# Optimization experiments

Measured on AMD Instinct MI355X. Metric: run time of the kernel, lower is better.

Reference implementation:

```python
import jax, jax.numpy as jnp
import numpy as np

TGT, BSZ, E = 2048, 4, 1024
NUM_HEADS = 16
HEAD_DIM = E // NUM_HEADS


def setup_inputs() -> dict:
    key = jax.random.key(0)
    ks = jax.random.split(key, 5)
    return {
        "query": jax.random.normal(ks[0], (TGT, BSZ, E), dtype=jnp.float32),
        "key": jax.random.normal(ks[1], (TGT, BSZ, E), dtype=jnp.float32),
        "value": jax.random.normal(ks[2], (TGT, BSZ, E), dtype=jnp.float32),
        "in_proj_weight": jax.random.normal(ks[3], (3 * E, E), dtype=jnp.float32) * (1.0 / np.sqrt(E)),
        "in_proj_bias": jnp.zeros((3 * E,), dtype=jnp.float32),
        "out_proj_weight": jax.random.normal(ks[4], (E, E), dtype=jnp.float32) * (1.0 / np.sqrt(E)),
        "out_proj_bias": jnp.zeros((E,), dtype=jnp.float32),
    }


def reference(query, key, value, in_proj_weight, in_proj_bias, out_proj_weight, out_proj_bias):
    tgt_len, bsz, embed_dim = query.shape
    src_len = key.shape[0]
    h, hd = NUM_HEADS, embed_dim // NUM_HEADS

    w_q, w_k, w_v = jnp.split(in_proj_weight, 3, axis=0)
    b_q, b_k, b_v = jnp.split(in_proj_bias, 3, axis=0)
    q = query @ w_q.T + b_q   # (Nt, B, E)
    k = key @ w_k.T + b_k     # (Ns, B, E)
    v = value @ w_v.T + b_v

    # (L, B, E) -> (B*H, L, hd)
    q = q.reshape(tgt_len, bsz * h, hd).transpose(1, 0, 2)
    k = k.reshape(src_len, bsz * h, hd).transpose(1, 0, 2)
    v = v.reshape(src_len, bsz * h, hd).transpose(1, 0, 2)

    q = q / jnp.sqrt(jnp.asarray(hd, dtype=q.dtype))
    attn = jnp.einsum('bte,bse->bts', q, k)          # (B*H, Nt, Ns)
    attn = jax.nn.softmax(attn, axis=-1)
    out = jnp.einsum('bts,bse->bte', attn, v)        # (B*H, Nt, hd)

    out = out.transpose(1, 0, 2).reshape(tgt_len, bsz, embed_dim)
    out = out @ out_proj_weight.T + out_proj_bias    # (Nt, B, out_dim)

    avg_weights = attn.reshape(bsz, h, tgt_len, src_len).mean(axis=1)
    return (out, avg_weights)
```

## Files before the change

### kernel.cpp

```cpp
#include <hip/hip_runtime.h>
#include <hip/hip_bf16.h>
#include <hip/hip_fp16.h>

#define TGT 2048
#define BSZ 4
#define EMB 1024
#define NH  16
#define HD  64
#define NTOK (TGT*BSZ)
#define BH   (BSZ*NH)

typedef unsigned short u16;
typedef __attribute__((ext_vector_type(8))) short    s16x8;
typedef __attribute__((ext_vector_type(8))) _Float16 f16x8;
typedef __attribute__((ext_vector_type(2))) _Float16 f16x2;
typedef __attribute__((ext_vector_type(4))) float    f32x4;

#define MFMA_BF16(a,b,c) __builtin_amdgcn_mfma_f32_16x16x32_bf16(a,b,c,0,0,0)
#define MFMA_F16(a,b,c)  __builtin_amdgcn_mfma_f32_16x16x32_f16(a,b,c,0,0,0)

#define GLOAD_LDS16(gsrc, ldst) \
  __builtin_amdgcn_global_load_lds((const __attribute__((address_space(1))) unsigned int*)(gsrc), \
                                   (__attribute__((address_space(3))) unsigned int*)(ldst), 16, 0, 0)

__device__ __forceinline__ void split_one(float x, u16& h, u16& l) {
  __hip_bfloat16 hb = __float2bfloat16(x);
  float hf = __bfloat162float(hb);
  __hip_bfloat16 lb = __float2bfloat16(x - hf);
  h = *reinterpret_cast<u16*>(&hb);
  l = *reinterpret_cast<u16*>(&lb);
}

__global__ __launch_bounds__(256) void split_kernel(const float* __restrict__ x,
    u16* __restrict__ hi, u16* __restrict__ lo, int n4) {
  int i = blockIdx.x * 256 + threadIdx.x;
  if (i >= n4) return;
  float4 v = reinterpret_cast<const float4*>(x)[i];
  ushort4 h, l;
  split_one(v.x, h.x, l.x);
  split_one(v.y, h.y, l.y);
  split_one(v.z, h.z, l.z);
  split_one(v.w, h.w, l.w);
  reinterpret_cast<ushort4*>(hi)[i] = h;
  reinterpret_cast<ushort4*>(lo)[i] = l;
}

template<int EPI>
__global__ __launch_bounds__(256) void gemm_split(
    const u16* __restrict__ Ah, const u16* __restrict__ Al,
    const u16* __restrict__ Bh, const u16* __restrict__ Bl,
    const float* __restrict__ bias, float scale, void* __restrict__ outp, int K)
{
  __shared__ __align__(16) u16 As[128*64];
  __shared__ __align__(16) u16 Bs[128*64];
  const int tid  = threadIdx.x;
  const int bm0  = blockIdx.y * 128;
  const int bn0  = blockIdx.x * 128;
  const int wave = tid >> 6, lane = tid & 63, lr = lane & 15, lg = lane >> 4;

  f32x4 zero = {0.f, 0.f, 0.f, 0.f};
  f32x4 acc[2][8];
  #pragma unroll
  for (int i = 0; i < 2; i++)
    #pragma unroll
    for (int j = 0; j < 8; j++) acc[i][j] = zero;

  const u16* srcA[4];
  const u16* srcB[4];
  #pragma unroll
  for (int j = 0; j < 4; j++) {
    int gi  = tid + j*256;
    int row = gi >> 3;
    int lgc = (gi & 7) ^ (row & 7);
    const u16* baA = (lgc < 4) ? Ah : Al;
    const u16* baB = (lgc < 4) ? Bh : Bl;
    srcA[j] = baA + (size_t)(bm0 + row)*K + (lgc & 3)*8;
    srcB[j] = baB + (size_t)(bn0 + row)*K + (lgc & 3)*8;
  }
  char* AsB = (char*)As;
  char* BsB = (char*)Bs;
  const int ldsb = wave*1024;

  for (int kt = 0; kt < K; kt += 32) {
    __syncthreads();
    #pragma unroll
    for (int j = 0; j < 4; j++) {
      GLOAD_LDS16(srcA[j] + kt, AsB + ldsb + j*4096);
      GLOAD_LDS16(srcB[j] + kt, BsB + ldsb + j*4096);
    }
    __syncthreads();

    s16x8 ah[2], al2[2];
    #pragma unroll
    for (int mf = 0; mf < 2; mf++) {
      int row = wave*32 + mf*16 + lr;
      const char* rb = AsB + row*128;
      ah[mf]  = *(const s16x8*)(rb + (((lg    ) ^ (row & 7)) << 4));
      al2[mf] = *(const s16x8*)(rb + (((lg | 4) ^ (row & 7)) << 4));
    }
    #pragma unroll
    for (int nf = 0; nf < 8; nf++) {
      int row = nf*16 + lr;
      const char* rb = BsB + row*128;
      s16x8 bh8 = *(const s16x8*)(rb + (((lg    ) ^ (row & 7)) << 4));
      s16x8 bl8 = *(const s16x8*)(rb + (((lg | 4) ^ (row & 7)) << 4));
      #pragma unroll
      for (int mf = 0; mf < 2; mf++) {
        acc[mf][nf] = MFMA_BF16(al2[mf], bh8, acc[mf][nf]);
        acc[mf][nf] = MFMA_BF16(ah[mf],  bl8, acc[mf][nf]);
        acc[mf][nf] = MFMA_BF16(ah[mf],  bh8, acc[mf][nf]);
      }
    }
  }
  #pragma unroll
  for (int mf = 0; mf < 2; mf++)
    #pragma unroll
    for (int nf = 0; nf < 8; nf++)
      #pragma unroll
      for (int r = 0; r < 4; r++) {
        int m = bm0 + wave*32 + mf*16 + lg*4 + r;
        int n = bn0 + nf*16 + lr;
        float v = (acc[mf][nf][r] + bias[n]) * scale;
        if constexpr (EPI == 0) {
          int t = m >> 2, b = m & 3, h = n >> 6, d = n & 63;
          ((_Float16*)outp)[(size_t)((b*NH + h)*TGT + t)*HD + d] = (_Float16)v;
        } else if constexpr (EPI == 1) {
          int s = m >> 2, b = m & 3, h = n >> 6, d = n & 63;
          ((_Float16*)outp)[(size_t)((b*NH + h)*HD + d)*TGT + s] = (_Float16)v;
        } else {
          ((float*)outp)[(size_t)m*EMB + n] = v;
        }
      }
}

__global__ __launch_bounds__(256) void flash_kernel(
    const _Float16* __restrict__ Qf, const _Float16* __restrict__ Kf,
    const _Float16* __restrict__ Vt, u16* __restrict__ Oh, u16* __restrict__ Ol,
    float* __restrict__ lse)
{
  __shared__ __align__(16) _Float16 Qs[64][72];
  __shared__ __align__(16) _Float16 Ks[64][72];
  __shared__ __align__(16) _Float16 Vs[64][72];
  __shared__ __align__(16) _Float16 Ps[4][16][72];
  const int tid = threadIdx.x, wave = tid >> 6, lane = tid & 63, lr = lane & 15, lg = lane >> 4;
  const int bh = blockIdx.y, t0 = blockIdx.x * 64;
  const int b = bh >> 4, h = bh & 15;

  #pragma unroll
  for (int i = 0; i < 2; i++) {
    int c = tid + i*256, r = c >> 3, co = (c & 7) * 8;
    *(uint4*)&Qs[r][co] = *(const uint4*)&Qf[((size_t)bh*TGT + t0 + r)*HD + co];
  }
  float m_run = -1e30f, l_run = 0.f;
  f32x4 zero = {0.f, 0.f, 0.f, 0.f};
  f32x4 accO[4];
  #pragma unroll
  for (int i = 0; i < 4; i++) accO[i] = zero;

  for (int s0 = 0; s0 < TGT; s0 += 64) {
    __syncthreads();
    #pragma unroll
    for (int i = 0; i < 2; i++) {
      int c = tid + i*256, r = c >> 3, co = (c & 7) * 8;
      *(uint4*)&Ks[r][co] = *(const uint4*)&Kf[((size_t)bh*TGT + s0 + r)*HD + co];
      *(uint4*)&Vs[r][co] = *(const uint4*)&Vt[((size_t)bh*HD + r)*TGT + s0 + co];
    }
    __syncthreads();
    f32x4 sacc[4];
    #pragma unroll
    for (int sf = 0; sf < 4; sf++) sacc[sf] = zero;
    #pragma unroll
    for (int sf = 0; sf < 4; sf++)
      #pragma unroll
      for (int kf = 0; kf < 2; kf++) {
        f16x8 a = *(const f16x8*)&Ks[sf*16 + lr][kf*32 + lg*8];
        f16x8 q = *(const f16x8*)&Qs[wave*16 + lr][kf*32 + lg*8];
        sacc[sf] = MFMA_F16(a, q, sacc[sf]);
      }
    float pm = -1e30f;
    #pragma unroll
    for (int sf = 0; sf < 4; sf++)
      #pragma unroll
      for (int r = 0; r < 4; r++) pm = fmaxf(pm, sacc[sf][r]);
    pm = fmaxf(pm, __shfl_xor(pm, 16, 64));
    pm = fmaxf(pm, __shfl_xor(pm, 32, 64));
    float m_new = fmaxf(m_run, pm);
    float fsc = exp2f(m_run - m_new);
    float psum = 0.f;
    #pragma unroll
    for (int sf = 0; sf < 4; sf++)
      #pragma unroll
      for (int r = 0; r < 4; r++) {
        float p = exp2f(sacc[sf][r] - m_new);
        sacc[sf][r] = p;
        psum += p;
      }
    psum += __shfl_xor(psum, 16, 64);
    psum += __shfl_xor(psum, 32, 64);
    l_run = l_run * fsc + psum;
    m_run = m_new;
    #pragma unroll
    for (int sf = 0; sf < 4; sf++) {
      f16x2 p01 = { (_Float16)sacc[sf][0], (_Float16)sacc[sf][1] };
      f16x2 p23 = { (_Float16)sacc[sf][2], (_Float16)sacc[sf][3] };
      *(f16x2*)&Ps[wave][lr][sf*16 + lg*4]     = p01;
      *(f16x2*)&Ps[wave][lr][sf*16 + lg*4 + 2] = p23;
    }
    float fr[4];
    #pragma unroll
    for (int r = 0; r < 4; r++) fr[r] = __shfl(fsc, lg*4 + r, 64);
    #pragma unroll
    for (int df = 0; df < 4; df++) {
      accO[df][0] *= fr[0]; accO[df][1] *= fr[1];
      accO[df][2] *= fr[2]; accO[df][3] *= fr[3];
    }
    f16x8 pa0 = *(const f16x8*)&Ps[wave][lr][lg*8];
    f16x8 pa1 = *(const f16x8*)&Ps[wave][lr][32 + lg*8];
    #pragma unroll
    for (int df = 0; df < 4; df++) {
      f16x8 v0 = *(const f16x8*)&Vs[df*16 + lr][lg*8];
      f16x8 v1 = *(const f16x8*)&Vs[df*16 + lr][32 + lg*8];
      accO[df] = MFMA_F16(pa0, v0, accO[df]);
      accO[df] = MFMA_F16(pa1, v1, accO[df]);
    }
  }
  float linv = 1.f / l_run;
  float rl[4];
  #pragma unroll
  for (int r = 0; r < 4; r++) rl[r] = __shfl(linv, lg*4 + r, 64);
  #pragma unroll
  for (int df = 0; df < 4; df++)
    #pragma unroll
    for (int r = 0; r < 4; r++) {
      float o = accO[df][r] * rl[r];
      int t = t0 + wave*16 + lg*4 + r;
      int d = df*16 + lr;
      size_t idx = (size_t)(t*BSZ + b)*EMB + h*HD + d;
      u16 hh, ll;
      split_one(o, hh, ll);
      Oh[idx] = hh; Ol[idx] = ll;
    }
  if (lane < 16)
    lse[(size_t)bh*TGT + t0 + wave*16 + lane] = m_run + log2f(l_run);
}

__global__ __launch_bounds__(256) void avg_kernel(
    const _Float16* __restrict__ Qf, const _Float16* __restrict__ Kf,
    const float* __restrict__ lse, float* __restrict__ avgO)
{
  __shared__ __align__(16) _Float16 Qs[128][64];
  __shared__ __align__(16) _Float16 Ks[128][64];
  __shared__ float lses[NH][128];
  const int tid = threadIdx.x, wave = tid >> 6, lane = tid & 63, lr = lane & 15, lg = lane >> 4;

  int fid = blockIdx.x;
  int nid = (fid & 7) * 128 + (fid >> 3);
  int st = nid & 15, tt = (nid >> 4) & 15, b = nid >> 8;
  int s0 = st * 128, t0 = tt * 128;

  #pragma unroll
  for (int i = 0; i < 8; i++) {
    int idx = tid + i * 256;
    int hh = idx >> 7, t = idx & 127;
    lses[hh][t] = lse[(size_t)(b*NH + hh)*TGT + t0 + t];
  }

  f32x4 zero = {0.f, 0.f, 0.f, 0.f};
  f32x4 acc[2][8];
  #pragma unroll
  for (int i = 0; i < 2; i++)
    #pragma unroll
    for (int j = 0; j < 8; j++) acc[i][j] = zero;

  const int rQ = wave * 32;
  const int srcsub = (((lane & 7) ^ (lane >> 3)) << 4) + (lane >> 3) * 128;

  for (int h = 0; h < NH; h++) {
    __syncthreads();
    {
      const char* qb = (const char*)(Qf + ((size_t)(b*NH + h)*TGT + t0) * HD);
      const char* kb = (const char*)(Kf + ((size_t)(b*NH + h)*TGT + s0) * HD);
      const char* gb = (wave < 2) ? qb : kb;
      char* lb = (char*)((wave < 2) ? &Qs[0][0] : &Ks[0][0]);
      const int half = (wave & 1) * 8;
      #pragma unroll
      for (int j = 0; j < 8; j++) {
        int J = half + j;
        GLOAD_LDS16(gb + (size_t)J * 1024 + srcsub, lb + J * 1024);
      }
    }
    __syncthreads();

    float lsr[2][4];
    #pragma unroll
    for (int mf = 0; mf < 2; mf++)
      #pragma unroll
      for (int r = 0; r < 4; r++)
        lsr[mf][r] = lses[h][rQ + mf*16 + lg*4 + r];

    f16x8 aq[2][2];
    #pragma unroll
    for (int mf = 0; mf < 2; mf++)
      #pragma unroll
      for (int kf = 0; kf < 2; kf++) {
        int row = rQ + mf*16 + lr;
        int cb = ((kf*4 + lg) ^ (row & 7)) << 4;
        aq[mf][kf] = *(const f16x8*)((const char*)&Qs[0][0] + row*128 + cb);
      }
    #pragma unroll
    for (int nf = 0; nf < 8; nf++) {
      f32x4 s4[2] = {zero, zero};
      #pragma unroll
      for (int kf = 0; kf < 2; kf++) {
        int row = nf*16 + lr;
        int cb = ((kf*4 + lg) ^ (row & 7)) << 4;
        f16x8 bk = *(const f16x8*)((const char*)&Ks[0][0] + row*128 + cb);
        s4[0] = MFMA_F16(aq[0][kf], bk, s4[0]);
        s4[1] = MFMA_F16(aq[1][kf], bk, s4[1]);
      }
      #pragma unroll
      for (int mf = 0; mf < 2; mf++)
        #pragma unroll
        for (int r = 0; r < 4; r++)
          acc[mf][nf][r] += exp2f(s4[mf][r] - lsr[mf][r]);
    }
  }

  #pragma unroll
  for (int mf = 0; mf < 2; mf++)
    #pragma unroll
    for (int nf = 0; nf < 8; nf++)
      #pragma unroll
      for (int r = 0; r < 4; r++) {
        int t = t0 + rQ + mf*16 + lg*4 + r;
        int s = s0 + nf*16 + lr;
        avgO[((size_t)b*TGT + t)*TGT + s] = acc[mf][nf][r] * (1.f/16.f);
      }
}

extern "C" void kernel_launch(void* const* d_in, const int* in_sizes, int n_in,
                              void* d_out, int out_size, void* d_ws, size_t ws_size,
                              hipStream_t stream) {
  const float* query = (const float*)d_in[0];
  const float* key_  = (const float*)d_in[1];
  const float* value = (const float*)d_in[2];
  const float* ipw   = (const float*)d_in[3];
  const float* ipb   = (const float*)d_in[4];
  const float* opw   = (const float*)d_in[5];
  const float* opb   = (const float*)d_in[6];
  float* out = (float*)d_out;
  float* avg = out + (size_t)TGT*BSZ*EMB;

  char* ws = (char*)d_ws;
  size_t o = 0;
  auto alloc = [&](size_t bytes) { char* p = ws + o; o += bytes; return p; };
  u16* Wh  = (u16*)alloc((size_t)3*EMB*EMB*2);
  u16* Wl  = (u16*)alloc((size_t)3*EMB*EMB*2);
  u16* Woh = (u16*)alloc((size_t)EMB*EMB*2);
  u16* Wol = (u16*)alloc((size_t)EMB*EMB*2);
  u16* Xh  = (u16*)alloc((size_t)NTOK*EMB*2);
  u16* Xl  = (u16*)alloc((size_t)NTOK*EMB*2);
  _Float16* Qf = (_Float16*)alloc((size_t)NTOK*EMB*2);
  _Float16* Kf = (_Float16*)alloc((size_t)NTOK*EMB*2);
  _Float16* Vt = (_Float16*)alloc((size_t)NTOK*EMB*2);
  u16* OhA = (u16*)alloc((size_t)NTOK*EMB*2);
  u16* OlA = (u16*)alloc((size_t)NTOK*EMB*2);
  float* lseA = (float*)alloc((size_t)BH*TGT*4);
  (void)ws_size; (void)in_sizes; (void)n_in; (void)out_size;

  const float QSCALE = 0.18033688011112042f;

  split_kernel<<<3*EMB*EMB/1024, 256, 0, stream>>>(ipw, Wh, Wl, 3*EMB*EMB/4);
  split_kernel<<<EMB*EMB/1024, 256, 0, stream>>>(opw, Woh, Wol, EMB*EMB/4);

  dim3 ggrid(EMB/128, NTOK/128);
  split_kernel<<<NTOK*EMB/1024, 256, 0, stream>>>(query, Xh, Xl, NTOK*EMB/4);
  gemm_split<0><<<ggrid, 256, 0, stream>>>(Xh, Xl, Wh, Wl, ipb, QSCALE, (void*)Qf, EMB);
  split_kernel<<<NTOK*EMB/1024, 256, 0, stream>>>(key_, Xh, Xl, NTOK*EMB/4);
  gemm_split<0><<<ggrid, 256, 0, stream>>>(Xh, Xl, Wh + (size_t)EMB*EMB, Wl + (size_t)EMB*EMB,
                                           ipb + EMB, 1.0f, (void*)Kf, EMB);
  split_kernel<<<NTOK*EMB/1024, 256, 0, stream>>>(value, Xh, Xl, NTOK*EMB/4);
  gemm_split<1><<<ggrid, 256, 0, stream>>>(Xh, Xl, Wh + (size_t)2*EMB*EMB, Wl + (size_t)2*EMB*EMB,
                                           ipb + 2*EMB, 1.0f, (void*)Vt, EMB);

  flash_kernel<<<dim3(TGT/64, BH), 256, 0, stream>>>(Qf, Kf, Vt, OhA, OlA, lseA);
  avg_kernel<<<1024, 256, 0, stream>>>(Qf, Kf, lseA, avg);
  gemm_split<2><<<ggrid, 256, 0, stream>>>(OhA, OlA, Woh, Wol, opb, 1.0f, (void*)out, EMB);
}
```

Measured before the change: 714.0 us.

## Rewrite flash attention with 32x32 MFMA, register-resident Q, and permlane P exchange

The flash kernel now processes 128 query rows per block, with each wave owning 32 rows. It uses 32x32x16 f16 MFMAs, keeps Q fragments in registers instead of LDS, and loads K/V straight into XOR-swizzled LDS with global_load_lds. The P matrix is converted with pkrtz and rearranged through v_permlane32_swap rather than an LDS round-trip, so the per-row rescale needs no shuffles. The aim is to cut LDS traffic, shuffles and sync overhead in the attention inner loop, at the cost of more registers per thread and half as many blocks.

```diff
diff --git a/kernel.cpp b/kernel.cpp
--- a/kernel.cpp
+++ b/kernel.cpp
@@ -11,13 +11,17 @@
 #define BH   (BSZ*NH)
 
 typedef unsigned short u16;
-typedef __attribute__((ext_vector_type(8))) short    s16x8;
-typedef __attribute__((ext_vector_type(8))) _Float16 f16x8;
-typedef __attribute__((ext_vector_type(2))) _Float16 f16x2;
-typedef __attribute__((ext_vector_type(4))) float    f32x4;
-
-#define MFMA_BF16(a,b,c) __builtin_amdgcn_mfma_f32_16x16x32_bf16(a,b,c,0,0,0)
-#define MFMA_F16(a,b,c)  __builtin_amdgcn_mfma_f32_16x16x32_f16(a,b,c,0,0,0)
+typedef __attribute__((ext_vector_type(8)))  short        s16x8;
+typedef __attribute__((ext_vector_type(8)))  _Float16     f16x8;
+typedef __attribute__((ext_vector_type(2)))  _Float16     f16x2;
+typedef __attribute__((ext_vector_type(2)))  __fp16       fp16x2;
+typedef __attribute__((ext_vector_type(4)))  float        f32x4;
+typedef __attribute__((ext_vector_type(16))) float        f32x16;
+typedef __attribute__((ext_vector_type(4)))  unsigned int u32x4;
+
+#define MFMA_BF16(a,b,c)  __builtin_amdgcn_mfma_f32_16x16x32_bf16(a,b,c,0,0,0)
+#define MFMA_F16(a,b,c)   __builtin_amdgcn_mfma_f32_16x16x32_f16(a,b,c,0,0,0)
+#define MFMA32_F16(a,b,c) __builtin_amdgcn_mfma_f32_32x32x16_f16(a,b,c,0,0,0)
 
 #define GLOAD_LDS16(gsrc, ldst) \
   __builtin_amdgcn_global_load_lds((const __attribute__((address_space(1))) unsigned int*)(gsrc), \
@@ -138,110 +142,126 @@
     const _Float16* __restrict__ Vt, u16* __restrict__ Oh, u16* __restrict__ Ol,
     float* __restrict__ lse)
 {
-  __shared__ __align__(16) _Float16 Qs[64][72];
-  __shared__ __align__(16) _Float16 Ks[64][72];
-  __shared__ __align__(16) _Float16 Vs[64][72];
-  __shared__ __align__(16) _Float16 Ps[4][16][72];
-  const int tid = threadIdx.x, wave = tid >> 6, lane = tid & 63, lr = lane & 15, lg = lane >> 4;
-  const int bh = blockIdx.y, t0 = blockIdx.x * 64;
+  __shared__ __align__(16) _Float16 Ks[64*64];
+  __shared__ __align__(16) _Float16 Vs[64*64];
+  const int tid = threadIdx.x, wq = tid >> 6, lane = tid & 63;
+  const int lt = lane & 31, hl = lane >> 5;
+  const int bh = blockIdx.y, t0 = blockIdx.x * 128;
   const int b = bh >> 4, h = bh & 15;
-
-  #pragma unroll
-  for (int i = 0; i < 2; i++) {
-    int c = tid + i*256, r = c >> 3, co = (c & 7) * 8;
-    *(uint4*)&Qs[r][co] = *(const uint4*)&Qf[((size_t)bh*TGT + t0 + r)*HD + co];
-  }
+  const int t = t0 + wq*32 + lt;
+
+  f16x8 qf[4];
+  #pragma unroll
+  for (int kk = 0; kk < 4; kk++)
+    qf[kk] = *(const f16x8*)&Qf[((size_t)bh*TGT + t)*HD + kk*16 + hl*8];
+
   float m_run = -1e30f, l_run = 0.f;
-  f32x4 zero = {0.f, 0.f, 0.f, 0.f};
-  f32x4 accO[4];
-  #pragma unroll
-  for (int i = 0; i < 4; i++) accO[i] = zero;
+  f32x16 accO[2];
+  #pragma unroll
+  for (int i = 0; i < 16; i++) { accO[0][i] = 0.f; accO[1][i] = 0.f; }
+
+  char* KsB = (char*)Ks;
+  char* VsB = (char*)Vs;
 
   for (int s0 = 0; s0 < TGT; s0 += 64) {
     __syncthreads();
     #pragma unroll
-    for (int i = 0; i < 2; i++) {
-      int c = tid + i*256, r = c >> 3, co = (c & 7) * 8;
-      *(uint4*)&Ks[r][co] = *(const uint4*)&Kf[((size_t)bh*TGT + s0 + r)*HD + co];
-      *(uint4*)&Vs[r][co] = *(const uint4*)&Vt[((size_t)bh*HD + r)*TGT + s0 + co];
-    }
-    __syncthreads();
-    f32x4 sacc[4];
-    #pragma unroll
-    for (int sf = 0; sf < 4; sf++) sacc[sf] = zero;
-    #pragma unroll
-    for (int sf = 0; sf < 4; sf++)
-      #pragma unroll
-      for (int kf = 0; kf < 2; kf++) {
-        f16x8 a = *(const f16x8*)&Ks[sf*16 + lr][kf*32 + lg*8];
-        f16x8 q = *(const f16x8*)&Qs[wave*16 + lr][kf*32 + lg*8];
-        sacc[sf] = MFMA_F16(a, q, sacc[sf]);
-      }
+    for (int j = 0; j < 2; j++) {
+      int gi = tid + j*256;
+      int row = gi >> 3, sg = (gi & 7) ^ (row & 7);
+      GLOAD_LDS16(Kf + ((size_t)bh*TGT + s0 + row)*HD + sg*8, KsB + wq*1024 + j*4096);
+      GLOAD_LDS16(Vt + ((size_t)bh*HD + row)*TGT + s0 + sg*8, VsB + wq*1024 + j*4096);
+    }
+    __syncthreads();
+
+    f32x16 sacc[2];
+    #pragma unroll
+    for (int i = 0; i < 16; i++) { sacc[0][i] = 0.f; sacc[1][i] = 0.f; }
+    #pragma unroll
+    for (int sf = 0; sf < 2; sf++)
+      #pragma unroll
+      for (int kk = 0; kk < 4; kk++) {
+        int row = sf*32 + lt;
+        int g = (2*kk + hl) ^ (row & 7);
+        f16x8 kfr = *(const f16x8*)(KsB + row*128 + g*16);
+        sacc[sf] = MFMA32_F16(kfr, qf[kk], sacc[sf]);
+      }
+
     float pm = -1e30f;
     #pragma unroll
-    for (int sf = 0; sf < 4; sf++)
-      #pragma unroll
-      for (int r = 0; r < 4; r++) pm = fmaxf(pm, sacc[sf][r]);
-    pm = fmaxf(pm, __shfl_xor(pm, 16, 64));
+    for (int sf = 0; sf < 2; sf++)
+      #pragma unroll
+      for (int r = 0; r < 16; r++) pm = fmaxf(pm, sacc[sf][r]);
     pm = fmaxf(pm, __shfl_xor(pm, 32, 64));
     float m_new = fmaxf(m_run, pm);
     float fsc = exp2f(m_run - m_new);
     float psum = 0.f;
     #pragma unroll
-    for (int sf = 0; sf < 4; sf++)
-      #pragma unroll
-      for (int r = 0; r < 4; r++) {
+    for (int sf = 0; sf < 2; sf++)
+      #pragma unroll
+      for (int r = 0; r < 16; r++) {
         float p = exp2f(sacc[sf][r] - m_new);
         sacc[sf][r] = p;
         psum += p;
       }
-    psum += __shfl_xor(psum, 16, 64);
     psum += __shfl_xor(psum, 32, 64);
     l_run = l_run * fsc + psum;
     m_run = m_new;
-    #pragma unroll
-    for (int sf = 0; sf < 4; sf++) {
-      f16x2 p01 = { (_Float16)sacc[sf][0], (_Float16)sacc[sf][1] };
-      f16x2 p23 = { (_Float16)sacc[sf][2], (_Float16)sacc[sf][3] };
-      *(f16x2*)&Ps[wave][lr][sf*16 + lg*4]     = p01;
-      *(f16x2*)&Ps[wave][lr][sf*16 + lg*4 + 2] = p23;
-    }
-    float fr[4];
-    #pragma unroll
-    for (int r = 0; r < 4; r++) fr[r] = __shfl(fsc, lg*4 + r, 64);
-    #pragma unroll
-    for (int df = 0; df < 4; df++) {
-      accO[df][0] *= fr[0]; accO[df][1] *= fr[1];
-      accO[df][2] *= fr[2]; accO[df][3] *= fr[3];
-    }
-    f16x8 pa0 = *(const f16x8*)&Ps[wave][lr][lg*8];
-    f16x8 pa1 = *(const f16x8*)&Ps[wave][lr][32 + lg*8];
-    #pragma unroll
-    for (int df = 0; df < 4; df++) {
-      f16x8 v0 = *(const f16x8*)&Vs[df*16 + lr][lg*8];
-      f16x8 v1 = *(const f16x8*)&Vs[df*16 + lr][32 + lg*8];
-      accO[df] = MFMA_F16(pa0, v0, accO[df]);
-      accO[df] = MFMA_F16(pa1, v1, accO[df]);
+    accO[0] *= fsc;
+    accO[1] *= fsc;
+
+    #pragma unroll
+    for (int sf = 0; sf < 2; sf++) {
+      unsigned int P0[4], P1[4];
+      #pragma unroll
+      for (int q = 0; q < 4; q++) {
+        union { fp16x2 h2; unsigned int u; } c0, c1;
+        c0.h2 = __builtin_amdgcn_cvt_pkrtz(sacc[sf][4*q],     sacc[sf][4*q + 1]);
+        c1.h2 = __builtin_amdgcn_cvt_pkrtz(sacc[sf][4*q + 2], sacc[sf][4*q + 3]);
+        P0[q] = c0.u;
+        P1[q] = c1.u;
+      }
+      #pragma unroll
+      for (int mp = 0; mp < 2; mp++) {
+        unsigned int a0 = P0[2*mp], b0 = P0[2*mp + 1];
+        unsigned int a1 = P1[2*mp], b1 = P1[2*mp + 1];
+        asm("v_permlane32_swap_b32 %0, %1" : "+v"(a0), "+v"(b0));
+        asm("v_permlane32_swap_b32 %0, %1" : "+v"(a1), "+v"(b1));
+        union { u32x4 u; f16x8 f; } pw;
+        pw.u = (u32x4){a0, a1, b0, b1};
+        const int m = sf*2 + mp;
+        #pragma unroll
+        for (int df = 0; df < 2; df++) {
+          int row = df*32 + lt;
+          int g = (2*m + hl) ^ (row & 7);
+          f16x8 vfr = *(const f16x8*)(VsB + row*128 + g*16);
+          accO[df] = MFMA32_F16(vfr, pw.f, accO[df]);
+        }
+      }
     }
   }
+
   float linv = 1.f / l_run;
-  float rl[4];
-  #pragma unroll
-  for (int r = 0; r < 4; r++) rl[r] = __shfl(linv, lg*4 + r, 64);
-  #pragma unroll
-  for (int df = 0; df < 4; df++)
-    #pragma unroll
-    for (int r = 0; r < 4; r++) {
-      float o = accO[df][r] * rl[r];
-      int t = t0 + wave*16 + lg*4 + r;
-      int d = df*16 + lr;
-      size_t idx = (size_t)(t*BSZ + b)*EMB + h*HD + d;
-      u16 hh, ll;
-      split_one(o, hh, ll);
-      Oh[idx] = hh; Ol[idx] = ll;
-    }
-  if (lane < 16)
-    lse[(size_t)bh*TGT + t0 + wave*16 + lane] = m_run + log2f(l_run);
+  #pragma unroll
+  for (int df = 0; df < 2; df++)
+    #pragma unroll
+    for (int q = 0; q < 4; q++) {
+      ushort4 hs, ls;
+      float o0 = accO[df][4*q]     * linv;
+      float o1 = accO[df][4*q + 1] * linv;
+      float o2 = accO[df][4*q + 2] * linv;
+      float o3 = accO[df][4*q + 3] * linv;
+      split_one(o0, hs.x, ls.x);
+      split_one(o1, hs.y, ls.y);
+      split_one(o2, hs.z, ls.z);
+      split_one(o3, hs.w, ls.w);
+      int d0 = 32*df + 8*q + 4*hl;
+      size_t idx = ((size_t)t*BSZ + b)*EMB + h*HD + d0;
+      *(ushort4*)&Oh[idx] = hs;
+      *(ushort4*)&Ol[idx] = ls;
+    }
+  if (hl == 0)
+    lse[(size_t)bh*TGT + t] = m_run + log2f(l_run);
 }
 
 __global__ __launch_bounds__(256) void avg_kernel(
@@ -332,9 +352,9 @@
     for (int nf = 0; nf < 8; nf++)
       #pragma unroll
       for (int r = 0; r < 4; r++) {
-        int t = t0 + rQ + mf*16 + lg*4 + r;
-        int s = s0 + nf*16 + lr;
-        avgO[((size_t)b*TGT + t)*TGT + s] = acc[mf][nf][r] * (1.f/16.f);
+        int ti = t0 + rQ + mf*16 + lg*4 + r;
+        int sj = s0 + nf*16 + lr;
+        avgO[((size_t)b*TGT + ti)*TGT + sj] = acc[mf][nf][r] * (1.f/16.f);
       }
 }
 
@@ -383,7 +403,7 @@
   gemm_split<1><<<ggrid, 256, 0, stream>>>(Xh, Xl, Wh + (size_t)2*EMB*EMB, Wl + (size_t)2*EMB*EMB,
                                            ipb + 2*EMB, 1.0f, (void*)Vt, EMB);
 
-  flash_kernel<<<dim3(TGT/64, BH), 256, 0, stream>>>(Qf, Kf, Vt, OhA, OlA, lseA);
+  flash_kernel<<<dim3(TGT/128, BH), 256, 0, stream>>>(Qf, Kf, Vt, OhA, OlA, lseA);
   avg_kernel<<<1024, 256, 0, stream>>>(Qf, Kf, lseA, avg);
   gemm_split<2><<<ggrid, 256, 0, stream>>>(OhA, OlA, Woh, Wol, opb, 1.0f, (void*)out, EMB);
 }
```

New measurement: 666.3 us. 6.7% less time.
